# Optimization experiments

Hardware: AMD Instinct MI355X
Metric: run time of the kernel (lower is better)

The kernel has to match this reference:

```python
import jax, jax.numpy as jnp
import numpy as np

L, B, E, H = 512, 64, 512, 1024

def setup_inputs() -> dict:
    key = jax.random.key(0)
    ks = jax.random.split(key, 10)
    scale = 1.0 / np.sqrt(E + H)  # ~torch Linear init scale
    inp = {
        "x": jax.random.normal(ks[0], (L, B, E), dtype=jnp.float32),
        "c": jnp.zeros((B, H), dtype=jnp.float32),
        "h": jnp.zeros((B, H), dtype=jnp.float32),
    }
    names = ["Wf", "bf", "Wi", "bi", "Wg", "bg", "Wo", "bo"]
    for idx, name in enumerate(names):
        k = ks[idx + 1]
        if name.startswith("W"):
            inp[name] = jax.random.normal(k, (E + H, H), dtype=jnp.float32) * scale
        else:
            inp[name] = jax.random.normal(k, (H,), dtype=jnp.float32) * scale
    return inp


def reference(x, c, h, Wf, bf, Wi, bi, Wg, bg, Wo, bo):
    # Fuse the 4 gate projections into one GEMM: same math since all 4 gates
    # consume the identical concat([x_t, h_{t-1}]) input.
    W = jnp.concatenate([Wf, Wi, Wg, Wo], axis=1)  # (E+H, 4H)
    b = jnp.concatenate([bf, bi, bg, bo])          # (4H,)

    def step(carry, x_t):
        c_prev, h_prev = carry
        xh = jnp.concatenate([x_t, h_prev], axis=-1)       # (B, E+H)
        z = xh @ W + b                                     # (B, 4H)
        f_t, i_t, g_t, o_t = jnp.split(z, 4, axis=-1)
        f_t = jax.nn.sigmoid(f_t)
        i_t = jax.nn.sigmoid(i_t)
        g_t = jnp.tanh(g_t)
        o_t = jax.nn.sigmoid(o_t)
        c_t = c_prev * f_t + i_t * g_t
        h_t = o_t * jnp.tanh(c_t)
        return (c_t, h_t), (c_t, h_t)

    (_, _), (c_full, h_full) = jax.lax.scan(step, (c, h), x)
    return c_full, h_full
```

## Files before the change

kernel.cpp:

```cpp
#include <hip/hip_runtime.h>

typedef unsigned int u32;
typedef unsigned short u16;
using u32x4 = __attribute__((ext_vector_type(4))) u32;
using f16x8 = __attribute__((ext_vector_type(8))) _Float16;
using f32x4 = __attribute__((ext_vector_type(4))) float;

#define LT 512
#define BNB 64
#define ED 512
#define HD 1024
#define OUT_HALF_BYTES ((size_t)LT * BNB * HD * 4)

#define WXP_OFF  ((size_t)0)
#define WHP_OFF  ((size_t)(4u << 20))
#define BIAS_OFF ((size_t)(12u << 20))
#define HSTG_OFF ((size_t)((12u << 20) + (16u << 10)))
#define FLAG_OFF ((size_t)((12u << 20) + (16u << 10) + (512u << 10)))

__device__ __forceinline__ u16 f2h(float f) {
  _Float16 h = (_Float16)f;
  return __builtin_bit_cast(u16, h);
}
__device__ __forceinline__ float h2f(u16 s) {
  return (float)__builtin_bit_cast(_Float16, s);
}
__device__ __forceinline__ u32 pk2(float a, float b) {
  return (u32)f2h(a) | ((u32)f2h(b) << 16);
}
__device__ __forceinline__ void glds16(const void* g, void* l) {
  using GP = const __attribute__((address_space(1))) u32*;
  using SP = __attribute__((address_space(3))) u32*;
  __builtin_amdgcn_global_load_lds((GP)g, (SP)l, 16, 0, 0);
}
__device__ __forceinline__ f32x4 mfma_f16(f16x8 a, f16x8 b, f32x4 c) {
  return __builtin_amdgcn_mfma_f32_16x16x32_f16(a, b, c, 0, 0, 0);
}
__device__ __forceinline__ float sigm(float x) { return 1.0f / (1.0f + __expf(-x)); }
__device__ __forceinline__ float tanh_(float x) { return 2.0f / (1.0f + __expf(-2.0f * x)) - 1.0f; }

__device__ __forceinline__ u32x4 ldg16_cc(const void* p) {
  u32x4 r;
  asm volatile("global_load_dwordx4 %0, %1, off sc0 sc1" : "=v"(r) : "v"(p) : "memory");
  return r;
}
__device__ __forceinline__ u32 ld_flag_cc(const void* p) {
  u32 r;
  asm volatile("global_load_dword %0, %1, off sc0 sc1\n\ts_waitcnt vmcnt(0)"
               : "=v"(r) : "v"(p) : "memory");
  return r;
}
__device__ __forceinline__ void st_u16_cc(void* p, u32 v) {
  asm volatile("global_store_short %0, %1, off sc0 sc1" ::"v"(p), "v"(v) : "memory");
}
__device__ __forceinline__ void stg_u32_cc(void* p, u32 v) {
  asm volatile("global_store_dword %0, %1, off sc0 sc1" ::"v"(p), "v"(v) : "memory");
}
__device__ __forceinline__ u32 ldg_u16_plain(const void* p) {
  u32 r;
  asm volatile("global_load_ushort %0, %1, off" : "=v"(r) : "v"(p) : "memory");
  return r;
}
__device__ __forceinline__ void waitv0() { asm volatile("s_waitcnt vmcnt(0)" ::: "memory"); }


__global__ void pack_wx(const float* __restrict__ Wf, const float* __restrict__ Wi,
                        const float* __restrict__ Wg, const float* __restrict__ Wo,
                        u32x4* __restrict__ dst) {
  const int id = blockIdx.x * 256 + threadIdx.x;
  const int lane = id & 63;
  const int row = id >> 6;
  const int ntile = row >> 7;
  const int rem = row & 127;
  const int kt = rem >> 3;
  const int fn = rem & 7;
  const int np = (ntile << 7) + (fn << 4) + (lane & 15);
  const int g = (np >> 4) & 3;
  const int jfull = ((np >> 6) << 4) + (np & 15);
  const int k0 = (kt << 5) + ((lane >> 4) << 3);
  const float* W = (g == 0) ? Wf : (g == 1) ? Wi : (g == 2) ? Wg : Wo;
  const float* s = W + (size_t)k0 * HD + jfull;
  u16 h[8];
#pragma unroll
  for (int i = 0; i < 8; ++i) h[i] = f2h(s[(size_t)i * HD]);
  u32x4 v;
  v[0] = (u32)h[0] | ((u32)h[1] << 16);
  v[1] = (u32)h[2] | ((u32)h[3] << 16);
  v[2] = (u32)h[4] | ((u32)h[5] << 16);
  v[3] = (u32)h[6] | ((u32)h[7] << 16);
  dst[id] = v;
}

__global__ void pack_wh(const float* __restrict__ Wf, const float* __restrict__ Wi,
                        const float* __restrict__ Wg, const float* __restrict__ Wo,
                        u32x4* __restrict__ dst) {
  const int id = blockIdx.x * 256 + threadIdx.x;
  const int lane = id & 63;
  const int row = id >> 6;
  const int kk = row & 7;
  const int w = (row >> 3) & 3;
  const int nt = (row >> 5) & 7;
  const int cq = row >> 8;
  const int np = (cq << 7) + (nt << 4) + (lane & 15);
  const int g = (np >> 4) & 3;
  const int jfull = ((np >> 6) << 4) + (np & 15);
  const int k = ED + (w << 8) + (kk << 5) + ((lane >> 4) << 3);
  const float* W = (g == 0) ? Wf : (g == 1) ? Wi : (g == 2) ? Wg : Wo;
  const float* s = W + (size_t)k * HD + jfull;
  u16 h[8];
#pragma unroll
  for (int i = 0; i < 8; ++i) h[i] = f2h(s[(size_t)i * HD]);
  u32x4 v;
  v[0] = (u32)h[0] | ((u32)h[1] << 16);
  v[1] = (u32)h[2] | ((u32)h[3] << 16);
  v[2] = (u32)h[4] | ((u32)h[5] << 16);
  v[3] = (u32)h[6] | ((u32)h[7] << 16);
  dst[id] = v;
}

__global__ void pack_bias_flags(const float* __restrict__ bf, const float* __restrict__ bi,
                                const float* __restrict__ bg, const float* __restrict__ bo,
                                float* __restrict__ dst, int* __restrict__ flags) {
  const int id = blockIdx.x * 256 + threadIdx.x;
  if (id < 4096) {
    const int g = (id >> 4) & 3;
    const int jfull = ((id >> 6) << 4) + (id & 15);
    const float* B = (g == 0) ? bf : (g == 1) ? bi : (g == 2) ? bg : bo;
    dst[id] = B[jfull];
  }
  flags[id] = 0;
}


__global__ __launch_bounds__(256) void zx_gemm(const float* __restrict__ x,
                                               const u32x4* __restrict__ wxp,
                                               const float* __restrict__ biasp,
                                               char* __restrict__ outb) {
  __shared__ u32x4 Ab[512];
  __shared__ u32x4 Bb[512];
  const int bid = blockIdx.x;
  const int ntile = bid & 31;
  const int mtile = bid >> 5;
  const int tid = threadIdx.x;
  const int lane = tid & 63;
  const int wid = tid >> 6;
  const int wm = wid & 1;
  const int wn = wid >> 1;
  const int m0 = mtile << 7;

  const f32x4 fz = {0.f, 0.f, 0.f, 0.f};
  f32x4 acc[4][4];
#pragma unroll
  for (int i = 0; i < 4; ++i)
#pragma unroll
    for (int j = 0; j < 4; ++j) acc[i][j] = fz;

  for (int kt = 0; kt < 16; ++kt) {
#pragma unroll
    for (int r = 0; r < 2; ++r) {
      const int c = tid + (r << 8);
      const int fl = c & 63;
      const int fmg = c >> 6;
      const int row = m0 + (fmg << 4) + (fl & 15);
      const int kc = (kt << 5) + ((fl >> 4) << 3);
      const float* s = x + (size_t)row * ED + kc;
      const float4 p0 = *(const float4*)s;
      const float4 p1 = *(const float4*)(s + 4);
      u32x4 v;
      v[0] = pk2(p0.x, p0.y);
      v[1] = pk2(p0.z, p0.w);
      v[2] = pk2(p1.x, p1.y);
      v[3] = pk2(p1.z, p1.w);
      Ab[c] = v;
    }
    {
      const u32x4* bsrc = wxp + (((size_t)(ntile << 4) + kt) << 9);
#pragma unroll
      for (int r = 0; r < 2; ++r) {
        const int cb = (wid << 6) + (r << 8);
        glds16((const void*)(bsrc + cb + lane), (void*)&Bb[cb]);
      }
    }
    __syncthreads();
    f16x8 afr[4], bfr[4];
#pragma unroll
    for (int f = 0; f < 4; ++f) afr[f] = __builtin_bit_cast(f16x8, Ab[((wm * 4 + f) << 6) + lane]);
#pragma unroll
    for (int f = 0; f < 4; ++f) bfr[f] = __builtin_bit_cast(f16x8, Bb[((wn * 4 + f) << 6) + lane]);
#pragma unroll
    for (int fm = 0; fm < 4; ++fm)
#pragma unroll
      for (int fn = 0; fn < 4; ++fn) acc[fm][fn] = mfma_f16(afr[fm], bfr[fn], acc[fm][fn]);
    __syncthreads();
  }

  char* const cb_ = outb;
  char* const hb_ = outb + OUT_HALF_BYTES;
  const int r0 = (lane >> 4) << 2;
#pragma unroll
  for (int fn = 0; fn < 4; ++fn) {
    const int np = (ntile << 7) + (wn << 6) + (fn << 4) + (lane & 15);
    const float bv = biasp[np];
    const int gg = (np >> 4) & 3;
    const int cg = np >> 6;
    const int jj = np & 15;
    char* const outHalf = (gg < 2) ? cb_ : hb_;
    const size_t coloff = (size_t)(cg << 6) + ((gg & 1) << 5) + (jj << 1);
#pragma unroll
    for (int fm = 0; fm < 4; ++fm) {
#pragma unroll
      for (int r = 0; r < 4; ++r) {
        const int m = m0 + (wm << 6) + (fm << 4) + r0 + r;
        *(u16*)(outHalf + (size_t)m * 4096 + coloff) = f2h(acc[fm][fn][r] + bv);
      }
    }
  }
}


__global__ __launch_bounds__(256, 1) void lstm_rec(const float* __restrict__ c0,
                                                   const float* __restrict__ h0,
                                                   const u32x4* __restrict__ whp, char* outb,
                                                   u16* hstage, int* flags) {
  __shared__ float zb[4][8][16][17];
  const int bid = blockIdx.x;
  const int mslab = bid & 3;
  const int cq = bid >> 2;
  const int tid = threadIdx.x;
  const int lane = tid & 63;
  const int wid = tid >> 6;
  const int b_loc = tid >> 4;
  const int j_loc = tid & 15;
  const int b = (mslab << 4) + b_loc;
  const int col0 = (cq << 5) + j_loc;

  f16x8 wreg[8][8];
#pragma unroll
  for (int nt = 0; nt < 8; ++nt)
#pragma unroll
    for (int kk = 0; kk < 8; ++kk)
      wreg[nt][kk] = __builtin_bit_cast(
          f16x8, whp[((size_t)((cq << 8) + (nt << 5) + (wid << 3) + kk) << 6) + lane]);

  float creg0 = c0[(b << 10) + col0];
  float creg1 = c0[(b << 10) + col0 + 16];

  char* const cb_ = outb;
  char* const hb_ = outb + OUT_HALF_BYTES;

  u32 zx0[4], zx1[4];
  {
    const size_t rowb = ((size_t)b) << 12;
#pragma unroll
    for (int g = 0; g < 4; ++g) {
      const char* half = (g < 2) ? cb_ : hb_;
      zx0[g] = ldg_u16_plain(half + rowb + (cq << 7) + ((g & 1) << 5) + (j_loc << 1));
      zx1[g] = ldg_u16_plain(half + rowb + (cq << 7) + 64 + ((g & 1) << 5) + (j_loc << 1));
    }
  }
  st_u16_cc(hstage + (b << 10) + col0, (u32)f2h(h0[(b << 10) + col0]));
  st_u16_cc(hstage + (b << 10) + col0 + 16, (u32)f2h(h0[(b << 10) + col0 + 16]));
  waitv0();
  __syncthreads();
  if (tid == 0) stg_u32_cc(flags + (((mslab << 5) + cq) << 5), 1u);

  const u32 aoff = (u32)((((mslab << 4) + (lane & 15)) << 10) + (wid << 8) + ((lane >> 4) << 3));
  const int* const pf = flags + (((mslab << 5) + (lane & 31)) << 5);

  const f32x4 fz = {0.f, 0.f, 0.f, 0.f};
#pragma unroll 1
  for (int t = 0; t < LT; ++t) {
    u32 fl;
    do {
      fl = (u32)ld_flag_cc(pf);
    } while (!__all((int)(fl >= (u32)(t + 1))));

    const u16* ab = hstage + (((u32)t & 1) << 16) + aoff;
    u32x4 v[8];
#pragma unroll
    for (int kk = 0; kk < 8; ++kk) v[kk] = ldg16_cc(ab + (kk << 5));
    waitv0();
    __builtin_amdgcn_sched_barrier(0);

    f32x4 acc[8];
#pragma unroll
    for (int nt = 0; nt < 8; ++nt) acc[nt] = fz;
#pragma unroll
    for (int kk = 0; kk < 8; ++kk) {
      const f16x8 av = __builtin_bit_cast(f16x8, v[kk]);
#pragma unroll
      for (int nt = 0; nt < 8; ++nt) acc[nt] = mfma_f16(av, wreg[nt][kk], acc[nt]);
    }
    {
      const int rr = (lane >> 4) << 2;
      const int cc = lane & 15;
#pragma unroll
      for (int nt = 0; nt < 8; ++nt)
#pragma unroll
        for (int r = 0; r < 4; ++r) zb[wid][nt][rr + r][cc] = acc[nt][r];
    }
    __syncthreads();

    float hv0, hv1;
    {
      float z[4];
#pragma unroll
      for (int g = 0; g < 4; ++g) {
        float s = h2f((u16)zx0[g]);
#pragma unroll
        for (int w = 0; w < 4; ++w) s += zb[w][g][b_loc][j_loc];
        z[g] = s;
      }
      const float fg = sigm(z[0]), ig = sigm(z[1]), gg = tanh_(z[2]), og = sigm(z[3]);
      creg0 = creg0 * fg + ig * gg;
      hv0 = og * tanh_(creg0);
    }
    {
      float z[4];
#pragma unroll
      for (int g = 0; g < 4; ++g) {
        float s = h2f((u16)zx1[g]);
#pragma unroll
        for (int w = 0; w < 4; ++w) s += zb[w][4 + g][b_loc][j_loc];
        z[g] = s;
      }
      const float fg = sigm(z[0]), ig = sigm(z[1]), gg = tanh_(z[2]), og = sigm(z[3]);
      creg1 = creg1 * fg + ig * gg;
      hv1 = og * tanh_(creg1);
    }

    const size_t rowoff = ((size_t)((t << 6) + b)) << 12;
    *(float*)(cb_ + rowoff + ((size_t)col0 << 2)) = creg0;
    *(float*)(cb_ + rowoff + ((size_t)(col0 + 16) << 2)) = creg1;
    *(float*)(hb_ + rowoff + ((size_t)col0 << 2)) = hv0;
    *(float*)(hb_ + rowoff + ((size_t)(col0 + 16) << 2)) = hv1;
    {
      const int tn = (t + 1 < LT) ? t + 1 : t;
      const size_t rown = ((size_t)((tn << 6) + b)) << 12;
#pragma unroll
      for (int g = 0; g < 4; ++g) {
        const char* half = (g < 2) ? cb_ : hb_;
        zx0[g] = ldg_u16_plain(half + rown + (cq << 7) + ((g & 1) << 5) + (j_loc << 1));
        zx1[g] = ldg_u16_plain(half + rown + (cq << 7) + 64 + ((g & 1) << 5) + (j_loc << 1));
      }
    }

    u16* hdst = hstage + ((((u32)(t + 1)) & 1) << 16) + (b << 10) + col0;
    st_u16_cc(hdst, (u32)f2h(hv0));
    st_u16_cc(hdst + 16, (u32)f2h(hv1));
    waitv0();
    __syncthreads();
    if (tid == 0) stg_u32_cc(flags + (((mslab << 5) + cq) << 5), (u32)(t + 2));
  }
}

extern "C" void kernel_launch(void* const* d_in, const int* in_sizes, int n_in, void* d_out,
                              int out_size, void* d_ws, size_t ws_size, hipStream_t stream) {
  const float* x = (const float*)d_in[0];
  const float* c0 = (const float*)d_in[1];
  const float* h0 = (const float*)d_in[2];
  const float* Wf = (const float*)d_in[3];
  const float* bf = (const float*)d_in[4];
  const float* Wi = (const float*)d_in[5];
  const float* bi = (const float*)d_in[6];
  const float* Wg = (const float*)d_in[7];
  const float* bg = (const float*)d_in[8];
  const float* Wo = (const float*)d_in[9];
  const float* bo = (const float*)d_in[10];

  char* ws = (char*)d_ws;
  u32x4* wxp = (u32x4*)(ws + WXP_OFF);
  u32x4* whp = (u32x4*)(ws + WHP_OFF);
  float* bp = (float*)(ws + BIAS_OFF);
  u16* hstage = (u16*)(ws + HSTG_OFF);
  int* flags = (int*)(ws + FLAG_OFF);

  pack_wx<<<1024, 256, 0, stream>>>(Wf, Wi, Wg, Wo, wxp);
  pack_wh<<<2048, 256, 0, stream>>>(Wf, Wi, Wg, Wo, whp);
  pack_bias_flags<<<32, 256, 0, stream>>>(bf, bi, bg, bo, bp, flags);
  zx_gemm<<<8192, 256, 0, stream>>>(x, wxp, bp, (char*)d_out);
  lstm_rec<<<128, 256, 0, stream>>>(c0, h0, whp, (char*)d_out, hstage, flags);
}
```

Baseline: 2.401 ms.

## Pipeline flag polling, pack flags densely, and defer output stores past the signal

Flag polling now keeps two outstanding loads in flight and waits for only one at a time, which shortens the gap between a flag becoming visible and the poll seeing it. Flags move from 128-byte spacing to a dense packed array, so one wavefront's poll touches fewer cache lines, at the risk of false sharing between writers. The c/h output stores and the next step's zx prefetch move after the flag release, so they no longer sit on the critical path before signalling. The LDS padding also changes from 17 to 18.

```diff
diff --git a/kernel.cpp b/kernel.cpp
--- a/kernel.cpp
+++ b/kernel.cpp
@@ -44,12 +44,6 @@
   asm volatile("global_load_dwordx4 %0, %1, off sc0 sc1" : "=v"(r) : "v"(p) : "memory");
   return r;
 }
-__device__ __forceinline__ u32 ld_flag_cc(const void* p) {
-  u32 r;
-  asm volatile("global_load_dword %0, %1, off sc0 sc1\n\ts_waitcnt vmcnt(0)"
-               : "=v"(r) : "v"(p) : "memory");
-  return r;
-}
 __device__ __forceinline__ void st_u16_cc(void* p, u32 v) {
   asm volatile("global_store_short %0, %1, off sc0 sc1" ::"v"(p), "v"(v) : "memory");
 }
@@ -60,6 +54,9 @@
   u32 r;
   asm volatile("global_load_ushort %0, %1, off" : "=v"(r) : "v"(p) : "memory");
   return r;
+}
+__device__ __forceinline__ void stg_f32_plain(void* p, float v) {
+  asm volatile("global_store_dword %0, %1, off" ::"v"(p), "v"(v) : "memory");
 }
 __device__ __forceinline__ void waitv0() { asm volatile("s_waitcnt vmcnt(0)" ::: "memory"); }
 
@@ -131,7 +128,6 @@
   flags[id] = 0;
 }
 
-
 __global__ __launch_bounds__(256) void zx_gemm(const float* __restrict__ x,
                                                const u32x4* __restrict__ wxp,
                                                const float* __restrict__ biasp,
@@ -222,7 +218,7 @@
                                                    const float* __restrict__ h0,
                                                    const u32x4* __restrict__ whp, char* outb,
                                                    u16* hstage, int* flags) {
-  __shared__ float zb[4][8][16][17];
+  __shared__ float zb[4][8][16][18];
   const int bid = blockIdx.x;
   const int mslab = bid & 3;
   const int cq = bid >> 2;
@@ -262,18 +258,28 @@
   st_u16_cc(hstage + (b << 10) + col0 + 16, (u32)f2h(h0[(b << 10) + col0 + 16]));
   waitv0();
   __syncthreads();
-  if (tid == 0) stg_u32_cc(flags + (((mslab << 5) + cq) << 5), 1u);
+  if (tid == 0) stg_u32_cc(flags + (mslab << 5) + cq, 1u);
 
   const u32 aoff = (u32)((((mslab << 4) + (lane & 15)) << 10) + (wid << 8) + ((lane >> 4) << 3));
-  const int* const pf = flags + (((mslab << 5) + (lane & 31)) << 5);
+  const int* const pfl = flags + (mslab << 5) + (lane & 31);
 
   const f32x4 fz = {0.f, 0.f, 0.f, 0.f};
 #pragma unroll 1
   for (int t = 0; t < LT; ++t) {
-    u32 fl;
-    do {
-      fl = (u32)ld_flag_cc(pf);
-    } while (!__all((int)(fl >= (u32)(t + 1))));
+    const u32 want = (u32)(t + 1);
+    u32 f0, f1;
+    asm volatile("global_load_dword %0, %1, off sc0 sc1" : "=v"(f0) : "v"(pfl) : "memory");
+    asm volatile("global_load_dword %0, %1, off sc0 sc1" : "=v"(f1) : "v"(pfl) : "memory");
+    for (;;) {
+      asm volatile("s_waitcnt vmcnt(1)" ::: "memory");
+      __builtin_amdgcn_sched_barrier(0);
+      if (__all((int)(f0 >= want))) break;
+      asm volatile("global_load_dword %0, %1, off sc0 sc1" : "=v"(f0) : "v"(pfl) : "memory");
+      asm volatile("s_waitcnt vmcnt(1)" ::: "memory");
+      __builtin_amdgcn_sched_barrier(0);
+      if (__all((int)(f1 >= want))) break;
+      asm volatile("global_load_dword %0, %1, off sc0 sc1" : "=v"(f1) : "v"(pfl) : "memory");
+    }
 
     const u16* ab = hstage + (((u32)t & 1) << 16) + aoff;
     u32x4 v[8];
@@ -327,22 +333,6 @@
       const float fg = sigm(z[0]), ig = sigm(z[1]), gg = tanh_(z[2]), og = sigm(z[3]);
       creg1 = creg1 * fg + ig * gg;
       hv1 = og * tanh_(creg1);
-    }
-
-    const size_t rowoff = ((size_t)((t << 6) + b)) << 12;
-    *(float*)(cb_ + rowoff + ((size_t)col0 << 2)) = creg0;
-    *(float*)(cb_ + rowoff + ((size_t)(col0 + 16) << 2)) = creg1;
-    *(float*)(hb_ + rowoff + ((size_t)col0 << 2)) = hv0;
-    *(float*)(hb_ + rowoff + ((size_t)(col0 + 16) << 2)) = hv1;
-    {
-      const int tn = (t + 1 < LT) ? t + 1 : t;
-      const size_t rown = ((size_t)((tn << 6) + b)) << 12;
-#pragma unroll
-      for (int g = 0; g < 4; ++g) {
-        const char* half = (g < 2) ? cb_ : hb_;
-        zx0[g] = ldg_u16_plain(half + rown + (cq << 7) + ((g & 1) << 5) + (j_loc << 1));
-        zx1[g] = ldg_u16_plain(half + rown + (cq << 7) + 64 + ((g & 1) << 5) + (j_loc << 1));
-      }
     }
 
     u16* hdst = hstage + ((((u32)(t + 1)) & 1) << 16) + (b << 10) + col0;
@@ -350,7 +340,23 @@
     st_u16_cc(hdst + 16, (u32)f2h(hv1));
     waitv0();
     __syncthreads();
-    if (tid == 0) stg_u32_cc(flags + (((mslab << 5) + cq) << 5), (u32)(t + 2));
+    if (tid == 0) stg_u32_cc(flags + (mslab << 5) + cq, (u32)(t + 2));
+
+    const size_t rowoff = ((size_t)((t << 6) + b)) << 12;
+    stg_f32_plain(cb_ + rowoff + ((size_t)col0 << 2), creg0);
+    stg_f32_plain(cb_ + rowoff + ((size_t)(col0 + 16) << 2), creg1);
+    stg_f32_plain(hb_ + rowoff + ((size_t)col0 << 2), hv0);
+    stg_f32_plain(hb_ + rowoff + ((size_t)(col0 + 16) << 2), hv1);
+    {
+      const int tn = (t + 1 < LT) ? t + 1 : t;
+      const size_t rown = ((size_t)((tn << 6) + b)) << 12;
+#pragma unroll
+      for (int g = 0; g < 4; ++g) {
+        const char* half = (g < 2) ? cb_ : hb_;
+        zx0[g] = ldg_u16_plain(half + rown + (cq << 7) + ((g & 1) << 5) + (j_loc << 1));
+        zx1[g] = ldg_u16_plain(half + rown + (cq << 7) + 64 + ((g & 1) << 5) + (j_loc << 1));
+      }
+    }
   }
 }
 
```

Measured after the change: 2.418 ms. Within noise of the previous version (+0.7%).
